# Performance work log

Hardware: AMD Instinct MI355X
Metric: run time of the kernel (lower is better)

## Reference

```python
import jax, jax.numpy as jnp
import numpy as np
from math import sqrt

B, T, C, H = 4, 2048, 1024, 16
D = C // H  # head dim = 64


def setup_inputs() -> dict:
    key = jax.random.key(0)
    ks = jax.random.split(key, 9)
    s = 1.0 / sqrt(C)
    return {
        "x": jax.random.normal(ks[0], (B, T, C), dtype=jnp.float32),
        "Wk": jax.random.normal(ks[1], (C, C), dtype=jnp.float32) * s,
        "bk": jax.random.normal(ks[2], (C,), dtype=jnp.float32) * 0.01,
        "Wq": jax.random.normal(ks[3], (C, C), dtype=jnp.float32) * s,
        "bq": jax.random.normal(ks[4], (C,), dtype=jnp.float32) * 0.01,
        "Wv": jax.random.normal(ks[5], (C, C), dtype=jnp.float32) * s,
        "bv": jax.random.normal(ks[6], (C,), dtype=jnp.float32) * 0.01,
        "Wp": jax.random.normal(ks[7], (C, C), dtype=jnp.float32) * s,
        "bp": jax.random.normal(ks[8], (C,), dtype=jnp.float32) * 0.01,
    }


def reference(x, Wk, bk, Wq, bq, Wv, bv, Wp, bp):
    # Linear projections, split into heads: [B, H, T, D]
    def heads(y):
        return y.reshape(B, T, H, D).transpose(0, 2, 1, 3)

    k = heads(x @ Wk + bk)
    q = heads(x @ Wq + bq)
    v = heads(x @ Wv + bv)

    # scaled dot-product attention with causal mask (dropout p=0 -> identity)
    attn = jnp.einsum("bhtd,bhsd->bhts", q, k) / jnp.sqrt(jnp.float32(D))
    causal = jnp.tril(jnp.ones((T, T), dtype=bool))
    attn = jnp.where(causal[None, None], attn, -jnp.inf)
    attn = jax.nn.softmax(attn, axis=-1)

    y = jnp.einsum("bhts,bhsd->bhtd", attn, v)  # [B, H, T, D]
    y = y.transpose(0, 2, 1, 3).reshape(B, T, C)
    return y @ Wp + bp
```

## Files before the change

kernel.cpp:

```cpp
#include <hip/hip_runtime.h>
#include <hip/hip_bf16.h>
#include <math.h>


typedef short bf16x8 __attribute__((ext_vector_type(8)));
typedef float f32x4 __attribute__((ext_vector_type(4)));
typedef _Float16 f16x4 __attribute__((ext_vector_type(4)));

__device__ __forceinline__ short f2b(float f) {
    unsigned u = __float_as_uint(f);
    u = (u + 0x7fffu + ((u >> 16) & 1u)) >> 16;
    return (short)u;
}
__device__ __forceinline__ float b2f(short s) {
    return __uint_as_float(((unsigned)(unsigned short)s) << 16);
}

__global__ __launch_bounds__(256) void prep_kernel(const float* __restrict__ x, short* __restrict__ xb,
                                                   const float* W0, const float* W1,
                                                   const float* W2, const float* W3,
                                                   short* O0, short* O1, short* O2, short* O3) {
    int tid = threadIdx.x;
    if (blockIdx.x < 8192) {
        int idx = blockIdx.x * 256 + tid;
        float4 v = ((const float4*)x)[idx];
        short4 o;
        o.x = f2b(v.x); o.y = f2b(v.y); o.z = f2b(v.z); o.w = f2b(v.w);
        ((short4*)xb)[idx] = o;
        return;
    }
    int wid = blockIdx.x - 8192;
    const float* W; short* O;
    switch (wid >> 8) {
        case 0: W = W0; O = O0; break;
        case 1: W = W1; O = O1; break;
        case 2: W = W2; O = O2; break;
        default: W = W3; O = O3; break;
    }
    int rem = wid & 255;
    int n0 = (rem >> 4) * 64, k0 = (rem & 15) * 64;
    __shared__ __align__(16) float Ls[64 * 68];
    #pragma unroll
    for (int it = 0; it < 4; ++it) {
        int c = tid + it * 256;
        int r = c >> 4, off = (c & 15) * 4;
        *(float4*)&Ls[r * 68 + off] = *(const float4*)&W[(k0 + r) * 1024 + n0 + off];
    }
    __syncthreads();
    #pragma unroll
    for (int it = 0; it < 2; ++it) {
        int c = tid + it * 256;
        int n = c >> 3, koff = (c & 7) * 8;
        union { short s[8]; int4 v; } u;
        #pragma unroll
        for (int k = 0; k < 8; ++k) u.s[k] = f2b(Ls[(koff + k) * 68 + n]);
        *(int4*)&O[(n0 + n) * 1024 + k0 + koff] = u.v;
    }
}

template<int MODE>
__global__ __launch_bounds__(512, 2) void gemm8_kernel(const short* __restrict__ A,
                                                       const short* Bt0, const short* Bt1, const short* Bt2,
                                                       const float* b0, const float* b1, const float* b2,
                                                       float s0, float s1, float s2,
                                                       void* O0, void* O1, void* O2) {
    int z = blockIdx.z;
    const short* Bt   = (z == 0) ? Bt0 : (z == 1) ? Bt1 : Bt2;
    const float* bias = (z == 0) ? b0  : (z == 1) ? b1  : b2;
    float scl         = (z == 0) ? s0  : (z == 1) ? s1  : s2;
    void* Out         = (z == 0) ? O0  : (z == 1) ? O1  : O2;

    __shared__ __align__(16) short lds[73728];

    int tid = threadIdx.x;
    int w = tid >> 6, lane = tid & 63, quad = lane >> 4, l15 = lane & 15;
    int m0 = blockIdx.x * 128, n0 = blockIdx.y * 256;

    int srccol = ((lane & 3) * 8) ^ ((lane & 32) ? 16 : 0);
    const short* pA0 = A  + (m0 + w * 16 + (lane >> 2)) * 1024 + srccol;
    const short* pA1 = pA0 + 32;
    const short* pB0 = Bt + (n0 + (2 * w) * 16 + (lane >> 2)) * 1024 + srccol;
    const short* pB1 = pB0 + 32;
    const short* pB2 = pB0 + 16 * 1024;
    const short* pB3 = pB2 + 32;

    int dA = (w * 2) * 512;
    int dB = 24576 + (w * 4) * 512;

    int offR = l15 * 64 + ((quad * 16) ^ ((l15 & 8) << 2));
    int ma4 = (w >> 2) * 4;
    int nb2 = (w & 3) * 2;
    int jrow0 = nb2, jrow1 = nb2 + 1, jrow2 = nb2 + 8, jrow3 = nb2 + 9;
    const char* ldsb = (const char*)lds;

    f32x4 acc[4][4] = {};
    bf16x8 afA[4], bfA[4], afB[4], bfB[4];

#define STG(p, off) __builtin_amdgcn_global_load_lds( \
        (const __attribute__((address_space(1))) unsigned int*)(p), \
        (__attribute__((address_space(3))) unsigned int*)&lds[off], 16, 0, 0)
#define RD(base, row, kk) (*(const bf16x8*)(ldsb + (base) + ((row) * 2 + (kk)) * 1024 + offR))

    STG(pA0,      dA);                 STG(pA1,      dA + 512);
    STG(pB0,      dB);                 STG(pB1,      dB + 512);
    STG(pB2,      dB + 1024);          STG(pB3,      dB + 1536);
    STG(pA0 + 64, 8192 + dA);          STG(pA1 + 64, 8192 + dA + 512);
    STG(pB0 + 64, 16384 + dB);         STG(pB1 + 64, 16384 + dB + 512);
    STG(pB2 + 64, 16384 + dB + 1024);  STG(pB3 + 64, 16384 + dB + 1536);
    asm volatile("s_waitcnt vmcnt(6)" ::: "memory");
    __builtin_amdgcn_s_barrier();
    __builtin_amdgcn_sched_barrier(0);

    #pragma unroll
    for (int i = 0; i < 4; ++i) afA[i] = RD(0, ma4 + i, 0);
    bfA[0] = RD(49152, jrow0, 0); bfA[1] = RD(49152, jrow1, 0);
    bfA[2] = RD(49152, jrow2, 0); bfA[3] = RD(49152, jrow3, 0);

    #pragma unroll
    for (int t = 0; t < 16; ++t) {
        const int rs  = t % 3;
        const int rs1 = (t + 1) % 3;
        const int ss  = (t + 2) % 3;
        const int Ar  = rs * 16384;
        const int Br  = 49152 + rs * 32768;
        const int Ar1 = rs1 * 16384;
        const int Br1 = 49152 + rs1 * 32768;

        #pragma unroll
        for (int i = 0; i < 4; ++i) afB[i] = RD(Ar, ma4 + i, 1);
        bfB[0] = RD(Br, jrow0, 1); bfB[1] = RD(Br, jrow1, 1);
        bfB[2] = RD(Br, jrow2, 1); bfB[3] = RD(Br, jrow3, 1);
        if (t + 2 < 16) {
            STG(pA0 + (t + 2) * 64, ss * 8192 + dA);
            STG(pA1 + (t + 2) * 64, ss * 8192 + dA + 512);
            STG(pB0 + (t + 2) * 64, ss * 16384 + dB);
        }
        asm volatile("s_waitcnt lgkmcnt(8)" ::: "memory");
        __builtin_amdgcn_sched_barrier(0);
        __builtin_amdgcn_s_setprio(1);
        #pragma unroll
        for (int i = 0; i < 4; ++i)
            #pragma unroll
            for (int j = 0; j < 4; ++j)
                acc[i][j] = __builtin_amdgcn_mfma_f32_16x16x32_bf16(afA[i], bfA[j], acc[i][j], 0, 0, 0);
        __builtin_amdgcn_s_setprio(0);
        if (t < 14) {
            asm volatile("s_waitcnt vmcnt(3)" ::: "memory");
        } else if (t == 14) {
            asm volatile("s_waitcnt vmcnt(0)" ::: "memory");
        }
        __builtin_amdgcn_s_barrier();
        __builtin_amdgcn_sched_barrier(0);

        if (t < 15) {
            #pragma unroll
            for (int i = 0; i < 4; ++i) afA[i] = RD(Ar1, ma4 + i, 0);
            bfA[0] = RD(Br1, jrow0, 0); bfA[1] = RD(Br1, jrow1, 0);
            bfA[2] = RD(Br1, jrow2, 0); bfA[3] = RD(Br1, jrow3, 0);
        }
        if (t + 2 < 16) {
            STG(pB1 + (t + 2) * 64, ss * 16384 + dB + 512);
            STG(pB2 + (t + 2) * 64, ss * 16384 + dB + 1024);
            STG(pB3 + (t + 2) * 64, ss * 16384 + dB + 1536);
        }
        if (t < 15) {
            asm volatile("s_waitcnt lgkmcnt(8)" ::: "memory");
        } else {
            asm volatile("s_waitcnt lgkmcnt(0)" ::: "memory");
        }
        __builtin_amdgcn_sched_barrier(0);
        __builtin_amdgcn_s_setprio(1);
        #pragma unroll
        for (int i = 0; i < 4; ++i)
            #pragma unroll
            for (int j = 0; j < 4; ++j)
                acc[i][j] = __builtin_amdgcn_mfma_f32_16x16x32_bf16(afB[i], bfB[j], acc[i][j], 0, 0, 0);
        __builtin_amdgcn_s_setprio(0);
        if (t < 15) {
            __builtin_amdgcn_s_barrier();
            __builtin_amdgcn_sched_barrier(0);
        }
    }
#undef STG
#undef RD

    int mrow = m0 + (w >> 2) * 64;
    int ncol = n0 + (w & 3) * 32;
    #pragma unroll
    for (int i = 0; i < 4; ++i) {
        #pragma unroll
        for (int j = 0; j < 4; ++j) {
            int gn = ncol + (j >> 1) * 128 + (j & 1) * 16 + l15;
            float bv = bias[gn];
            if (MODE == 0 && z == 2) {
                int gm0 = mrow + i * 16 + quad * 4;
                int b = gm0 >> 11, tt = gm0 & 2047, h = gn >> 6, d = gn & 63;
                f16x4 hv;
                #pragma unroll
                for (int r = 0; r < 4; ++r) hv[r] = (_Float16)((acc[i][j][r] + bv) * scl);
                *(f16x4*)&((_Float16*)Out)[((b * 16 + h) * 64 + d) * 2048 + tt] = hv;
            } else {
                #pragma unroll
                for (int r = 0; r < 4; ++r) {
                    int gm = mrow + i * 16 + quad * 4 + r;
                    float v = (acc[i][j][r] + bv) * scl;
                    if (MODE == 0) {
                        int b = gm >> 11, tt = gm & 2047, h = gn >> 6, d = gn & 63;
                        ((short*)Out)[(((b * 16 + h) * 2048) + tt) * 64 + d] = f2b(v);
                    } else {
                        ((float*)Out)[gm * 1024 + gn] = v;
                    }
                }
            }
        }
    }
}

__global__ __launch_bounds__(256, 3) void attn_kernel(const short* __restrict__ Q,
                                                      const short* __restrict__ K,
                                                      const _Float16* __restrict__ Vt,
                                                      short* __restrict__ Y) {
    __shared__ __align__(16) short    Ks[2][128 * 64];
    __shared__ __align__(16) _Float16 Vs[64 * 128];

    int tid = threadIdx.x;
    int w = tid >> 6, lane = tid & 63, quad = lane >> 4, l15 = lane & 15;
    int idx = blockIdx.x;
    int qi = 15 - (idx >> 6);
    int bh = idx & 63;

    const short* Qh = Q + bh * 2048 * 64;
    const short* Kh = K + bh * 2048 * 64;
    const _Float16* Vh = Vt + bh * 64 * 2048;

    bf16x8 qf[2][2];
    #pragma unroll
    for (int i = 0; i < 2; ++i)
        #pragma unroll
        for (int kh = 0; kh < 2; ++kh) {
            int t = qi * 128 + w * 32 + i * 16 + l15;
            qf[i][kh] = *(const bf16x8*)&Qh[t * 64 + kh * 32 + quad * 8];
        }

    int krow = lane >> 3;
    int kchunk = ((lane & 7) ^ krow) * 8;
    int vrow = lane >> 4;
    int vchunk = ((lane & 15) ^ (w * 4 + vrow)) * 8;

    int t7 = l15 & 7;
    int kf0_off = ((quad ^ t7) * 8);
    int kf1_off = (((quad + 4) ^ t7) * 8);
    int vsub = (quad & 1) * 4;
    int vchi = quad >> 1;

    f32x4 o[2][4] = {};
    float lsum[2] = {0.f, 0.f};

#define STGK(si_, buf_) do { \
    const short* Kt_ = Kh + (si_) * 128 * 64; \
    _Pragma("unroll") \
    for (int it = 0; it < 4; ++it) { \
        int kr0 = it * 32 + w * 8; \
        __builtin_amdgcn_global_load_lds( \
            (const __attribute__((address_space(1))) unsigned int*)&Kt_[(kr0 + krow) * 64 + kchunk], \
            (__attribute__((address_space(3))) unsigned int*)&Ks[buf_][kr0 * 64], 16, 0, 0); \
    } } while (0)
#define STGV(si_) do { \
    const _Float16* Vp_ = Vh + (si_) * 128; \
    _Pragma("unroll") \
    for (int it = 0; it < 4; ++it) { \
        int vr0 = it * 16 + w * 4; \
        __builtin_amdgcn_global_load_lds( \
            (const __attribute__((address_space(1))) unsigned int*)&Vp_[(vr0 + vrow) * 2048 + vchunk], \
            (__attribute__((address_space(3))) unsigned int*)&Vs[vr0 * 128], 16, 0, 0); \
    } } while (0)

    STGK(0, 0);
    STGV(0);

    for (int si = 0; si <= qi; ++si) {
        asm volatile("s_waitcnt vmcnt(0)" ::: "memory");
        __builtin_amdgcn_s_barrier();
        __builtin_amdgcn_sched_barrier(0);

        if (si < qi) STGK(si + 1, (si + 1) & 1);

        const short* Ksb = Ks[si & 1];
        bool diag = (si == qi);

        #pragma unroll
        for (int j = 0; j < 8; ++j) {
            int trow = (j * 16 + l15) * 64;
            bf16x8 kf0 = *(const bf16x8*)&Ksb[trow + kf0_off];
            bf16x8 kf1 = *(const bf16x8*)&Ksb[trow + kf1_off];
            f16x4 pfv[2];
            #pragma unroll
            for (int i = 0; i < 2; ++i) {
                f32x4 a = {};
                a = __builtin_amdgcn_mfma_f32_16x16x32_bf16(kf0, qf[i][0], a, 0, 0, 0);
                a = __builtin_amdgcn_mfma_f32_16x16x32_bf16(kf1, qf[i][1], a, 0, 0, 0);
                if (diag) {
                    int qrel = w * 32 + i * 16 + l15;
                    #pragma unroll
                    for (int r = 0; r < 4; ++r)
                        if (j * 16 + quad * 4 + r > qrel) a[r] = -1e30f;
                }
                float p0 = __builtin_amdgcn_exp2f(a[0]);
                float p1 = __builtin_amdgcn_exp2f(a[1]);
                float p2 = __builtin_amdgcn_exp2f(a[2]);
                float p3 = __builtin_amdgcn_exp2f(a[3]);
                lsum[i] += (p0 + p1) + (p2 + p3);
                pfv[i][0] = (_Float16)p0;
                pfv[i][1] = (_Float16)p1;
                pfv[i][2] = (_Float16)p2;
                pfv[i][3] = (_Float16)p3;
            }
            int vc = (j * 2 + vchi);
            #pragma unroll
            for (int mt = 0; mt < 4; ++mt) {
                int d = mt * 16 + l15;
                f16x4 vf = *(const f16x4*)&Vs[d * 128 + ((vc ^ l15) * 8) + vsub];
                o[0][mt] = __builtin_amdgcn_mfma_f32_16x16x16f16(vf, pfv[0], o[0][mt], 0, 0, 0);
                o[1][mt] = __builtin_amdgcn_mfma_f32_16x16x16f16(vf, pfv[1], o[1][mt], 0, 0, 0);
            }
        }

        if (si < qi) {
            asm volatile("s_waitcnt lgkmcnt(0)" ::: "memory");
            __builtin_amdgcn_s_barrier();
            __builtin_amdgcn_sched_barrier(0);
            STGV(si + 1);
        }
    }
#undef STGK
#undef STGV

    int b = bh >> 4, h = bh & 15;
    #pragma unroll
    for (int i = 0; i < 2; ++i) {
        float l = lsum[i];
        l += __shfl_xor(l, 16);
        l += __shfl_xor(l, 32);
        float rinv = 1.0f / l;
        int q = qi * 128 + w * 32 + i * 16 + l15;
        short* yrow = &Y[(b * 2048 + q) * 1024 + h * 64];
        #pragma unroll
        for (int mt = 0; mt < 4; ++mt) {
            short4 s4;
            s4.x = f2b(o[i][mt][0] * rinv);
            s4.y = f2b(o[i][mt][1] * rinv);
            s4.z = f2b(o[i][mt][2] * rinv);
            s4.w = f2b(o[i][mt][3] * rinv);
            *(short4*)&yrow[mt * 16 + quad * 4] = s4;
        }
    }
}

extern "C" void kernel_launch(void* const* d_in, const int* in_sizes, int n_in,
                              void* d_out, int out_size, void* d_ws, size_t ws_size,
                              hipStream_t stream) {
    const float* x  = (const float*)d_in[0];
    const float* Wk = (const float*)d_in[1];
    const float* bk = (const float*)d_in[2];
    const float* Wq = (const float*)d_in[3];
    const float* bq = (const float*)d_in[4];
    const float* Wv = (const float*)d_in[5];
    const float* bv = (const float*)d_in[6];
    const float* Wp = (const float*)d_in[7];
    const float* bp = (const float*)d_in[8];

    char* ws = (char*)d_ws;
    short*     xb  = (short*)(ws + 0);
    short*     Wqt = (short*)(ws + 16777216);
    short*     Wkt = (short*)(ws + 18874368);
    short*     Wvt = (short*)(ws + 20971520);
    short*     Wpt = (short*)(ws + 23068672);
    short*     Qb  = (short*)(ws + 25165824);
    short*     Kb  = (short*)(ws + 41943040);
    _Float16*  Vtb = (_Float16*)(ws + 75497472);
    short*     Yb  = (short*)(ws + 92274688);

    prep_kernel<<<9216, 256, 0, stream>>>(x, xb, Wq, Wk, Wv, Wp, Wqt, Wkt, Wvt, Wpt);
    gemm8_kernel<0><<<dim3(64, 4, 3), 512, 0, stream>>>(xb, Wqt, Wkt, Wvt, bq, bk, bv,
                                                        0.18033688011112042f , 1.0f, 1.0f,
                                                        (void*)Qb, (void*)Kb, (void*)Vtb);
    attn_kernel<<<1024, 256, 0, stream>>>(Qb, Kb, Vtb, Yb);
    gemm8_kernel<1><<<dim3(64, 4, 1), 512, 0, stream>>>(Yb, Wpt, nullptr, nullptr,
                                                        bp, nullptr, nullptr,
                                                        1.0f, 1.0f, 1.0f,
                                                        (void*)d_out, nullptr, nullptr);
}
```

Baseline: 238.7 us.

## Use 256-row query tiles with persistent atomic work queue in attention

The attention kernel now handles 256 query rows per block instead of 128, with each wave holding four 16-row slices. This halves how often each staged K/V tile is reloaded, since more queries share it. Blocks become persistent: they pull work items from a global atomic counter (heaviest items first), and the counter is cleared by a memset before launch. P values are also packed to fp16 with cvt_pkrtz. The trade-offs are higher register pressure from doubled accumulators, longer per-item critical paths with coarser load balance (512 items across 768 blocks), and an extra memset launch.

Result: slower. 524.0 us (+119.5%).

```diff
diff --git a/kernel.cpp b/kernel.cpp
--- a/kernel.cpp
+++ b/kernel.cpp
@@ -6,6 +6,7 @@
 typedef short bf16x8 __attribute__((ext_vector_type(8)));
 typedef float f32x4 __attribute__((ext_vector_type(4)));
 typedef _Float16 f16x4 __attribute__((ext_vector_type(4)));
+typedef __fp16 fp16x2 __attribute__((ext_vector_type(2)));
 
 __device__ __forceinline__ short f2b(float f) {
     unsigned u = __float_as_uint(f);
@@ -219,28 +220,14 @@
 __global__ __launch_bounds__(256, 3) void attn_kernel(const short* __restrict__ Q,
                                                       const short* __restrict__ K,
                                                       const _Float16* __restrict__ Vt,
-                                                      short* __restrict__ Y) {
+                                                      short* __restrict__ Y,
+                                                      int* __restrict__ ctr) {
     __shared__ __align__(16) short    Ks[2][128 * 64];
     __shared__ __align__(16) _Float16 Vs[64 * 128];
+    __shared__ int sh_item;
 
     int tid = threadIdx.x;
     int w = tid >> 6, lane = tid & 63, quad = lane >> 4, l15 = lane & 15;
-    int idx = blockIdx.x;
-    int qi = 15 - (idx >> 6);
-    int bh = idx & 63;
-
-    const short* Qh = Q + bh * 2048 * 64;
-    const short* Kh = K + bh * 2048 * 64;
-    const _Float16* Vh = Vt + bh * 64 * 2048;
-
-    bf16x8 qf[2][2];
-    #pragma unroll
-    for (int i = 0; i < 2; ++i)
-        #pragma unroll
-        for (int kh = 0; kh < 2; ++kh) {
-            int t = qi * 128 + w * 32 + i * 16 + l15;
-            qf[i][kh] = *(const bf16x8*)&Qh[t * 64 + kh * 32 + quad * 8];
-        }
 
     int krow = lane >> 3;
     int kchunk = ((lane & 7) ^ krow) * 8;
@@ -253,8 +240,29 @@
     int vsub = (quad & 1) * 4;
     int vchi = quad >> 1;
 
-    f32x4 o[2][4] = {};
-    float lsum[2] = {0.f, 0.f};
+    for (;;) {
+        if (tid == 0) sh_item = atomicAdd(ctr, 1);
+        __syncthreads();
+        int item = sh_item;
+        if (item >= 512) break;
+        int qi = 7 - (item >> 6);
+        int bh = item & 63;
+
+        const short* Qh = Q + bh * 2048 * 64;
+        const short* Kh = K + bh * 2048 * 64;
+        const _Float16* Vh = Vt + bh * 64 * 2048;
+
+        bf16x8 qf[4][2];
+        #pragma unroll
+        for (int i = 0; i < 4; ++i)
+            #pragma unroll
+            for (int kh = 0; kh < 2; ++kh) {
+                int t = qi * 256 + w * 64 + i * 16 + l15;
+                qf[i][kh] = *(const bf16x8*)&Qh[t * 64 + kh * 32 + quad * 8];
+            }
+
+        f32x4 o[4][4] = {};
+        float lsum[4] = {0.f, 0.f, 0.f, 0.f};
 
 #define STGK(si_, buf_) do { \
     const short* Kt_ = Kh + (si_) * 128 * 64; \
@@ -275,83 +283,88 @@
             (__attribute__((address_space(3))) unsigned int*)&Vs[vr0 * 128], 16, 0, 0); \
     } } while (0)
 
-    STGK(0, 0);
-    STGV(0);
-
-    for (int si = 0; si <= qi; ++si) {
-        asm volatile("s_waitcnt vmcnt(0)" ::: "memory");
-        __builtin_amdgcn_s_barrier();
-        __builtin_amdgcn_sched_barrier(0);
-
-        if (si < qi) STGK(si + 1, (si + 1) & 1);
-
-        const short* Ksb = Ks[si & 1];
-        bool diag = (si == qi);
-
-        #pragma unroll
-        for (int j = 0; j < 8; ++j) {
-            int trow = (j * 16 + l15) * 64;
-            bf16x8 kf0 = *(const bf16x8*)&Ksb[trow + kf0_off];
-            bf16x8 kf1 = *(const bf16x8*)&Ksb[trow + kf1_off];
-            f16x4 pfv[2];
-            #pragma unroll
-            for (int i = 0; i < 2; ++i) {
-                f32x4 a = {};
-                a = __builtin_amdgcn_mfma_f32_16x16x32_bf16(kf0, qf[i][0], a, 0, 0, 0);
-                a = __builtin_amdgcn_mfma_f32_16x16x32_bf16(kf1, qf[i][1], a, 0, 0, 0);
-                if (diag) {
-                    int qrel = w * 32 + i * 16 + l15;
-                    #pragma unroll
-                    for (int r = 0; r < 4; ++r)
-                        if (j * 16 + quad * 4 + r > qrel) a[r] = -1e30f;
-                }
-                float p0 = __builtin_amdgcn_exp2f(a[0]);
-                float p1 = __builtin_amdgcn_exp2f(a[1]);
-                float p2 = __builtin_amdgcn_exp2f(a[2]);
-                float p3 = __builtin_amdgcn_exp2f(a[3]);
-                lsum[i] += (p0 + p1) + (p2 + p3);
-                pfv[i][0] = (_Float16)p0;
-                pfv[i][1] = (_Float16)p1;
-                pfv[i][2] = (_Float16)p2;
-                pfv[i][3] = (_Float16)p3;
-            }
-            int vc = (j * 2 + vchi);
-            #pragma unroll
-            for (int mt = 0; mt < 4; ++mt) {
-                int d = mt * 16 + l15;
-                f16x4 vf = *(const f16x4*)&Vs[d * 128 + ((vc ^ l15) * 8) + vsub];
-                o[0][mt] = __builtin_amdgcn_mfma_f32_16x16x16f16(vf, pfv[0], o[0][mt], 0, 0, 0);
-                o[1][mt] = __builtin_amdgcn_mfma_f32_16x16x16f16(vf, pfv[1], o[1][mt], 0, 0, 0);
-            }
-        }
-
-        if (si < qi) {
-            asm volatile("s_waitcnt lgkmcnt(0)" ::: "memory");
+        STGK(0, 0);
+        STGV(0);
+
+        int nt = 2 * qi + 2;
+        for (int si = 0; si < nt; ++si) {
+            asm volatile("s_waitcnt vmcnt(0)" ::: "memory");
             __builtin_amdgcn_s_barrier();
             __builtin_amdgcn_sched_barrier(0);
-            STGV(si + 1);
-        }
-    }
+
+            if (si + 1 < nt) STGK(si + 1, (si + 1) & 1);
+
+            const short* Ksb = Ks[si & 1];
+            bool dz = (si >= 2 * qi);
+            int soff = (si - 2 * qi) * 128;
+
+            #pragma unroll
+            for (int j = 0; j < 8; ++j) {
+                int trow = (j * 16 + l15) * 64;
+                bf16x8 kf0 = *(const bf16x8*)&Ksb[trow + kf0_off];
+                bf16x8 kf1 = *(const bf16x8*)&Ksb[trow + kf1_off];
+                f16x4 pfv[4];
+                #pragma unroll
+                for (int i = 0; i < 4; ++i) {
+                    f32x4 a = {};
+                    a = __builtin_amdgcn_mfma_f32_16x16x32_bf16(kf0, qf[i][0], a, 0, 0, 0);
+                    a = __builtin_amdgcn_mfma_f32_16x16x32_bf16(kf1, qf[i][1], a, 0, 0, 0);
+                    if (dz) {
+                        int qrel = w * 64 + i * 16 + l15;
+                        #pragma unroll
+                        for (int r = 0; r < 4; ++r)
+                            if (soff + j * 16 + quad * 4 + r > qrel) a[r] = -1e30f;
+                    }
+                    float p0 = __builtin_amdgcn_exp2f(a[0]);
+                    float p1 = __builtin_amdgcn_exp2f(a[1]);
+                    float p2 = __builtin_amdgcn_exp2f(a[2]);
+                    float p3 = __builtin_amdgcn_exp2f(a[3]);
+                    lsum[i] += (p0 + p1) + (p2 + p3);
+                    union { fp16x2 h2[2]; f16x4 h4; } pu;
+                    pu.h2[0] = __builtin_amdgcn_cvt_pkrtz(p0, p1);
+                    pu.h2[1] = __builtin_amdgcn_cvt_pkrtz(p2, p3);
+                    pfv[i] = pu.h4;
+                }
+                int vc = (j * 2 + vchi);
+                #pragma unroll
+                for (int mt = 0; mt < 4; ++mt) {
+                    int d = mt * 16 + l15;
+                    f16x4 vf = *(const f16x4*)&Vs[d * 128 + ((vc ^ l15) * 8) + vsub];
+                    o[0][mt] = __builtin_amdgcn_mfma_f32_16x16x16f16(vf, pfv[0], o[0][mt], 0, 0, 0);
+                    o[1][mt] = __builtin_amdgcn_mfma_f32_16x16x16f16(vf, pfv[1], o[1][mt], 0, 0, 0);
+                    o[2][mt] = __builtin_amdgcn_mfma_f32_16x16x16f16(vf, pfv[2], o[2][mt], 0, 0, 0);
+                    o[3][mt] = __builtin_amdgcn_mfma_f32_16x16x16f16(vf, pfv[3], o[3][mt], 0, 0, 0);
+                }
+            }
+
+            if (si + 1 < nt) {
+                asm volatile("s_waitcnt lgkmcnt(0)" ::: "memory");
+                __builtin_amdgcn_s_barrier();
+                __builtin_amdgcn_sched_barrier(0);
+                STGV(si + 1);
+            }
+        }
 #undef STGK
 #undef STGV
 
-    int b = bh >> 4, h = bh & 15;
-    #pragma unroll
-    for (int i = 0; i < 2; ++i) {
-        float l = lsum[i];
-        l += __shfl_xor(l, 16);
-        l += __shfl_xor(l, 32);
-        float rinv = 1.0f / l;
-        int q = qi * 128 + w * 32 + i * 16 + l15;
-        short* yrow = &Y[(b * 2048 + q) * 1024 + h * 64];
-        #pragma unroll
-        for (int mt = 0; mt < 4; ++mt) {
-            short4 s4;
-            s4.x = f2b(o[i][mt][0] * rinv);
-            s4.y = f2b(o[i][mt][1] * rinv);
-            s4.z = f2b(o[i][mt][2] * rinv);
-            s4.w = f2b(o[i][mt][3] * rinv);
-            *(short4*)&yrow[mt * 16 + quad * 4] = s4;
+        int b = bh >> 4, h = bh & 15;
+        #pragma unroll
+        for (int i = 0; i < 4; ++i) {
+            float l = lsum[i];
+            l += __shfl_xor(l, 16);
+            l += __shfl_xor(l, 32);
+            float rinv = 1.0f / l;
+            int q = qi * 256 + w * 64 + i * 16 + l15;
+            short* yrow = &Y[(b * 2048 + q) * 1024 + h * 64];
+            #pragma unroll
+            for (int mt = 0; mt < 4; ++mt) {
+                short4 s4;
+                s4.x = f2b(o[i][mt][0] * rinv);
+                s4.y = f2b(o[i][mt][1] * rinv);
+                s4.z = f2b(o[i][mt][2] * rinv);
+                s4.w = f2b(o[i][mt][3] * rinv);
+                *(short4*)&yrow[mt * 16 + quad * 4] = s4;
+            }
         }
     }
 }
@@ -377,6 +390,7 @@
     short*     Wpt = (short*)(ws + 23068672);
     short*     Qb  = (short*)(ws + 25165824);
     short*     Kb  = (short*)(ws + 41943040);
+    int*       ctr = (int*)(ws + 58720256);
     _Float16*  Vtb = (_Float16*)(ws + 75497472);
     short*     Yb  = (short*)(ws + 92274688);
 
@@ -384,7 +398,8 @@
     gemm8_kernel<0><<<dim3(64, 4, 3), 512, 0, stream>>>(xb, Wqt, Wkt, Wvt, bq, bk, bv,
                                                         0.18033688011112042f , 1.0f, 1.0f,
                                                         (void*)Qb, (void*)Kb, (void*)Vtb);
-    attn_kernel<<<1024, 256, 0, stream>>>(Qb, Kb, Vtb, Yb);
+    hipMemsetAsync(ctr, 0, 4, stream);
+    attn_kernel<<<768, 256, 0, stream>>>(Qb, Kb, Vtb, Yb, ctr);
     gemm8_kernel<1><<<dim3(64, 4, 1), 512, 0, stream>>>(Yb, Wpt, nullptr, nullptr,
                                                         bp, nullptr, nullptr,
                                                         1.0f, 1.0f, 1.0f,
```
